# Performance work log

Measured on AMD Instinct MI355X. Metric: run time of the kernel, lower is better.

Reference implementation:

```python
import jax, jax.numpy as jnp
import numpy as np


def setup_inputs() -> dict:
    key = jax.random.key(0)
    k1, k2 = jax.random.split(key)
    B, C, H, W = 8, 64, 32, 32
    K = 8192
    x = jax.random.normal(k1, (B, C, H, W), dtype=jnp.float32)
    codebook = jax.random.normal(k2, (K, C), dtype=jnp.float32)
    return {"x": x, "codebook": codebook}


def reference(x, codebook):
    """Faithful JAX version of VQVAE.quantize().

    x:        [B, C, H, W] latent (output of pre_quant_conv)
    codebook: [K, C] embedding weight
    Returns (quant_out [B,C,H,W], commitment_loss, codebook_loss, indices [B,H,W]).
    """
    B, C, H, W = x.shape
    # [B, H, W, C] -> [B, N, C]
    xf = jnp.transpose(x, (0, 2, 3, 1)).reshape(B, H * W, C)

    # Squared pairwise distances (argmin of cdist == argmin of squared dist).
    x2 = jnp.sum(xf * xf, axis=-1, keepdims=True)            # [B, N, 1]
    e2 = jnp.sum(codebook * codebook, axis=-1)               # [K]
    xe = jnp.einsum('bnc,kc->bnk', xf, codebook)             # [B, N, K]
    d2 = x2 + e2[None, None, :] - 2.0 * xe                   # [B, N, K]
    idx = jnp.argmin(d2, axis=-1)                            # [B, N]

    quant = codebook[idx.reshape(-1)]                        # [B*N, C]
    xflat = xf.reshape(-1, C)                                # [B*N, C]

    commitment_loss = jnp.mean((jax.lax.stop_gradient(quant) - xflat) ** 2)
    codebook_loss = jnp.mean((quant - jax.lax.stop_gradient(xflat)) ** 2)

    # Straight-through estimator.
    quant_st = xflat + jax.lax.stop_gradient(quant - xflat)
    quant_out = jnp.transpose(quant_st.reshape(B, H, W, C), (0, 3, 1, 2))
    indices = idx.reshape(B, H, W)
    return quant_out, commitment_loss, codebook_loss, indices
```

## Files before the change

kernel.cpp:

```cpp
#include <hip/hip_runtime.h>


#define N_PTS   8192
#define K_CODES 8192
#define C_DIM   64
#define HWSZ    1024
#define QOUT_N  524288
#define SPLITS  32

#define WS_XS    0
#define WS_CBS   3145728
#define WS_E2H   6291456
#define WS_PACK  6324224
#define WS_PART  8421376

typedef __attribute__((ext_vector_type(8))) short short8;
typedef __attribute__((ext_vector_type(4))) float floatx4;

__device__ __forceinline__ unsigned short bf16_rne(float f) {
    unsigned u = __float_as_uint(f);
    return (unsigned short)((u + 0x7FFFu + ((u >> 16) & 1u)) >> 16);
}
__device__ __forceinline__ float bf16_val(unsigned short h) {
    return __uint_as_float(((unsigned)h) << 16);
}
__device__ __forceinline__ void split3(float v, unsigned short& h,
                                       unsigned short& m, unsigned short& l) {
    h = bf16_rne(v);
    float r1 = v - bf16_val(h);
    m = bf16_rne(r1);
    float r2 = r1 - bf16_val(m);
    l = bf16_rne(r2);
}
__device__ __forceinline__ void cp16(const void* g, void* l) {
    __builtin_amdgcn_global_load_lds(
        (const __attribute__((address_space(1))) void*)g,
        (__attribute__((address_space(3))) void*)l, 16, 0, 0);
}
__device__ __forceinline__ void cp4(const void* g, void* l) {
    __builtin_amdgcn_global_load_lds(
        (const __attribute__((address_space(1))) void*)g,
        (__attribute__((address_space(3))) void*)l, 4, 0, 0);
}

__global__ __launch_bounds__(256)
void vq_prep_kernel(const float* __restrict__ x,
                    const float* __restrict__ cb,
                    unsigned short* __restrict__ xS,
                    unsigned short* __restrict__ cbS,
                    float* __restrict__ e2h)
{
    const int bx  = blockIdx.x;
    const int tid = threadIdx.x;

    if (bx < 32) {
        const int k = bx * 256 + tid;
        const float* row = cb + k * C_DIM;
        float s = 0.0f;
        #pragma unroll
        for (int g = 0; g < 8; ++g) {
            float4 a = *(const float4*)(row + g * 8);
            float4 b = *(const float4*)(row + g * 8 + 4);
            float vv[8] = {a.x, a.y, a.z, a.w, b.x, b.y, b.z, b.w};
            unsigned short h8[8], m8[8], l8[8];
            #pragma unroll
            for (int j = 0; j < 8; ++j) {
                s = fmaf(vv[j], vv[j], s);
                split3(vv[j], h8[j], m8[j], l8[j]);
            }
            *(uint4*)(cbS + ((size_t)(0 * 8 + g) * 8192 + k) * 8) = *(const uint4*)h8;
            *(uint4*)(cbS + ((size_t)(1 * 8 + g) * 8192 + k) * 8) = *(const uint4*)m8;
            *(uint4*)(cbS + ((size_t)(2 * 8 + g) * 8192 + k) * 8) = *(const uint4*)l8;
        }
        e2h[k] = 0.5f * s;
    } else {
        const int u = bx - 32;
        const int b = u >> 3, g = u & 7;
        const float* xb = x + (size_t)(b * C_DIM + g * 8) * HWSZ;
        float v[4][8];
        #pragma unroll
        for (int cq = 0; cq < 8; ++cq) {
            float4 t4 = *(const float4*)(xb + cq * HWSZ + tid * 4);
            v[0][cq] = t4.x; v[1][cq] = t4.y; v[2][cq] = t4.z; v[3][cq] = t4.w;
        }
        #pragma unroll
        for (int j = 0; j < 4; ++j) {
            unsigned short h8[8], m8[8], l8[8];
            #pragma unroll
            for (int cq = 0; cq < 8; ++cq)
                split3(v[j][cq], h8[cq], m8[cq], l8[cq]);
            const size_t n = (size_t)b * 1024 + tid * 4 + j;
            *(uint4*)(xS + ((size_t)(0 * 8 + g) * 8192 + n) * 8) = *(const uint4*)h8;
            *(uint4*)(xS + ((size_t)(1 * 8 + g) * 8192 + n) * 8) = *(const uint4*)m8;
            *(uint4*)(xS + ((size_t)(2 * 8 + g) * 8192 + n) * 8) = *(const uint4*)l8;
        }
    }
}

#define SEG_SHORTS 512
#define BUF_SHORTS 12416

__device__ __forceinline__ void computeTileLDS(const short8 af[4][3][2],
                                               const unsigned short* __restrict__ bsrc,
                                               int tl, int quad, int col, int code,
                                               float bestv[4][4], int besti[4][4])
{
    short8 bf[3][2];
    #pragma unroll
    for (int p = 0; p < 3; ++p)
        #pragma unroll
        for (int s = 0; s < 2; ++s) {
            int seg = p * 8 + s * 4 + quad;
            bf[p][s] = *(const short8*)(bsrc + seg * SEG_SHORTS + (tl * 16 + col) * 8);
        }
    float me2 = -((const float*)(bsrc + 24 * SEG_SHORTS))[tl * 16 + col];

    floatx4 acc[4];
    #pragma unroll
    for (int t = 0; t < 4; ++t) acc[t] = (floatx4){me2, me2, me2, me2};

    #pragma unroll
    for (int s = 0; s < 2; ++s) {
        #pragma unroll
        for (int t = 0; t < 4; ++t)
            acc[t] = __builtin_amdgcn_mfma_f32_16x16x32_bf16(af[t][0][s], bf[0][s], acc[t], 0, 0, 0);
        #pragma unroll
        for (int t = 0; t < 4; ++t)
            acc[t] = __builtin_amdgcn_mfma_f32_16x16x32_bf16(af[t][0][s], bf[1][s], acc[t], 0, 0, 0);
        #pragma unroll
        for (int t = 0; t < 4; ++t)
            acc[t] = __builtin_amdgcn_mfma_f32_16x16x32_bf16(af[t][1][s], bf[0][s], acc[t], 0, 0, 0);
        #pragma unroll
        for (int t = 0; t < 4; ++t)
            acc[t] = __builtin_amdgcn_mfma_f32_16x16x32_bf16(af[t][0][s], bf[2][s], acc[t], 0, 0, 0);
        #pragma unroll
        for (int t = 0; t < 4; ++t)
            acc[t] = __builtin_amdgcn_mfma_f32_16x16x32_bf16(af[t][2][s], bf[0][s], acc[t], 0, 0, 0);
        #pragma unroll
        for (int t = 0; t < 4; ++t)
            acc[t] = __builtin_amdgcn_mfma_f32_16x16x32_bf16(af[t][1][s], bf[1][s], acc[t], 0, 0, 0);
    }

    #pragma unroll
    for (int t = 0; t < 4; ++t)
        #pragma unroll
        for (int r = 0; r < 4; ++r) {
            float sc = acc[t][r];
            bool gt = sc > bestv[t][r];
            bestv[t][r] = gt ? sc   : bestv[t][r];
            besti[t][r] = gt ? code : besti[t][r];
        }
}

__global__ __launch_bounds__(256, 2)
void vq_argmin_kernel(const unsigned short* __restrict__ xS,
                      const unsigned short* __restrict__ cbS,
                      const float* __restrict__ e2h,
                      unsigned long long* __restrict__ packedS)
{
    __shared__ __align__(16) unsigned short sBuf[2][BUF_SHORTS];

    const int tid   = threadIdx.x;
    const int lane  = tid & 63;
    const int w     = tid >> 6;
    const int col   = lane & 15;
    const int quad  = lane >> 4;
    const int mb    = blockIdx.x;
    const int split = blockIdx.y;
    const int m0    = mb * 256 + w * 64;
    const int nb0   = split * 256;

    short8 af[4][3][2];
    #pragma unroll
    for (int t = 0; t < 4; ++t) {
        int pt = m0 + t * 16 + col;
        #pragma unroll
        for (int p = 0; p < 3; ++p)
            #pragma unroll
            for (int s = 0; s < 2; ++s) {
                int g = s * 4 + quad;
                af[t][p][s] = *(const short8*)(xS + ((size_t)(p * 8 + g) * 8192 + pt) * 8);
            }
    }

    float bestv[4][4];
    int   besti[4][4];
    #pragma unroll
    for (int t = 0; t < 4; ++t)
        #pragma unroll
        for (int r = 0; r < 4; ++r) {
            bestv[t][r] = __uint_as_float(0xFF800000u);
            besti[t][r] = 0;
        }

    auto stage = [&](int k0, int buf) {
        unsigned short* dst = &sBuf[buf][0];
        #pragma unroll
        for (int i = 0; i < 6; ++i) {
            int f   = tid + i * 256;
            int seg = f >> 6;
            int l   = f & 63;
            cp16(cbS + ((size_t)seg * 8192 + k0 + l) * 8,
                 dst + seg * SEG_SHORTS + l * 8);
        }
        if (tid < 64)
            cp4(e2h + k0 + tid, (float*)(dst + 24 * SEG_SHORTS) + tid);
    };

    stage(nb0, 0);
    __syncthreads();

    for (int ch = 0; ch < 4; ++ch) {
        if (ch + 1 < 4) stage(nb0 + (ch + 1) * 64, (ch + 1) & 1);
        const unsigned short* bsrc = &sBuf[ch & 1][0];
        #pragma unroll
        for (int tl = 0; tl < 4; ++tl)
            computeTileLDS(af, bsrc, tl, quad, col,
                           nb0 + ch * 64 + tl * 16 + col, bestv, besti);
        __syncthreads();
    }

    unsigned long long* red = (unsigned long long*)&sBuf[0][0];
    #pragma unroll
    for (int t = 0; t < 4; ++t)
        #pragma unroll
        for (int r = 0; r < 4; ++r) {
            unsigned u = __float_as_uint(-bestv[t][r]);
            u = ((int)u < 0) ? ~u : (u | 0x80000000u);
            unsigned long long p = ((unsigned long long)u << 32) | (unsigned)besti[t][r];
            red[(w * 64 + t * 16 + quad * 4 + r) * 17 + col] = p;
        }
    __syncthreads();
    unsigned long long v = red[tid * 17];
    #pragma unroll
    for (int c = 1; c < 16; ++c) {
        unsigned long long q = red[tid * 17 + c];
        v = (q < v) ? q : v;
    }
    packedS[(size_t)split * N_PTS + mb * 256 + tid] = v;
}

__global__ __launch_bounds__(256)
void vq_gather_kernel(const float* __restrict__ x,
                      const float* __restrict__ cb,
                      const unsigned long long* __restrict__ packedS,
                      float* __restrict__ out,
                      float* __restrict__ part)
{
    __shared__ int sidx[64];
    const int tid  = threadIdx.x;
    const int lane = tid & 63;
    const int qd   = tid >> 6;
    const int n0   = blockIdx.x * 64;
    const int n    = n0 + lane;

    if (qd == 0) {
        unsigned long long v = packedS[n];
        #pragma unroll
        for (int s = 1; s < SPLITS; ++s) {
            unsigned long long q = packedS[(size_t)s * N_PTS + n];
            v = (q < v) ? q : v;
        }
        int idx = (int)(v & 0xFFFFFFFFull);
        sidx[lane] = idx;
        out[QOUT_N + 2 + n] = (float)idx;
    }
    __syncthreads();

    const int idx = sidx[lane];
    const int c0  = qd * 16;
    const int b   = n >> 10;
    const int hw  = n & 1023;
    const float* xb = x   + (size_t)b * (C_DIM * HWSZ) + hw;
    float*       ob = out + (size_t)b * (C_DIM * HWSZ) + hw;

    float s = 0.0f;
    #pragma unroll
    for (int c4 = 0; c4 < 4; ++c4) {
        float4 q = *(const float4*)(cb + (size_t)idx * C_DIM + c0 + c4 * 4);
        float qa[4] = {q.x, q.y, q.z, q.w};
        #pragma unroll
        for (int j = 0; j < 4; ++j) {
            int c = c0 + c4 * 4 + j;
            float xv = xb[c * HWSZ];
            float d  = qa[j] - xv;
            s = fmaf(d, d, s);
            ob[c * HWSZ] = xv + d;
        }
    }

    #pragma unroll
    for (int off = 32; off > 0; off >>= 1) s += __shfl_down(s, off, 64);
    if (lane == 0) part[blockIdx.x * 4 + qd] = s;
}

__global__ __launch_bounds__(256)
void vq_final_kernel(const float* __restrict__ part, float* __restrict__ out)
{
    __shared__ float w[4];
    float s = part[threadIdx.x] + part[threadIdx.x + 256];
    #pragma unroll
    for (int off = 32; off > 0; off >>= 1) s += __shfl_down(s, off, 64);
    if ((threadIdx.x & 63) == 0) w[threadIdx.x >> 6] = s;
    __syncthreads();
    if (threadIdx.x == 0) {
        float m = (w[0] + w[1] + w[2] + w[3]) * (1.0f / (float)QOUT_N);
        out[QOUT_N]     = m;
        out[QOUT_N + 1] = m;
    }
}

extern "C" void kernel_launch(void* const* d_in, const int* in_sizes, int n_in,
                              void* d_out, int out_size, void* d_ws, size_t ws_size,
                              hipStream_t stream)
{
    const float* x  = (const float*)d_in[0];
    const float* cb = (const float*)d_in[1];
    float* out = (float*)d_out;
    char*  ws  = (char*)d_ws;
    (void)ws_size;

    unsigned short* xS  = (unsigned short*)(ws + WS_XS);
    unsigned short* cbS = (unsigned short*)(ws + WS_CBS);
    float* e2h = (float*)(ws + WS_E2H);
    unsigned long long* packedS = (unsigned long long*)(ws + WS_PACK);
    float* part = (float*)(ws + WS_PART);

    vq_prep_kernel<<<96, 256, 0, stream>>>(x, cb, xS, cbS, e2h);
    vq_argmin_kernel<<<dim3(N_PTS / 256, SPLITS), 256, 0, stream>>>(xS, cbS, e2h, packedS);
    vq_gather_kernel<<<128, 256, 0, stream>>>(x, cb, packedS, out, part);
    vq_final_kernel<<<1, 256, 0, stream>>>(part, out);
}
```

Baseline: 103.8 us.

## Single-buffer codebook LDS staging and replace LDS reduction with wave shuffles

Replaces the double-buffered LDS staging of codebook chunks with a single buffer, loaded between two barriers after each chunk is computed. This halves LDS use per block so more blocks can be resident, at the cost of no longer overlapping chunk loads with MFMA compute. The final per-point argmin across the 16 columns now uses xor shuffles within the wave instead of an LDS scratch array and an extra barrier. Each lane writes the result for one point, computed from its column and quad.

```diff
diff --git a/kernel.cpp b/kernel.cpp
--- a/kernel.cpp
+++ b/kernel.cpp
@@ -158,7 +158,7 @@
                       const float* __restrict__ e2h,
                       unsigned long long* __restrict__ packedS)
 {
-    __shared__ __align__(16) unsigned short sBuf[2][BUF_SHORTS];
+    __shared__ __align__(16) unsigned short sBuf[BUF_SHORTS];
 
     const int tid   = threadIdx.x;
     const int lane  = tid & 63;
@@ -193,34 +193,35 @@
             besti[t][r] = 0;
         }
 
-    auto stage = [&](int k0, int buf) {
-        unsigned short* dst = &sBuf[buf][0];
+    auto stage = [&](int k0) {
         #pragma unroll
         for (int i = 0; i < 6; ++i) {
             int f   = tid + i * 256;
             int seg = f >> 6;
             int l   = f & 63;
             cp16(cbS + ((size_t)seg * 8192 + k0 + l) * 8,
-                 dst + seg * SEG_SHORTS + l * 8);
+                 sBuf + seg * SEG_SHORTS + l * 8);
         }
         if (tid < 64)
-            cp4(e2h + k0 + tid, (float*)(dst + 24 * SEG_SHORTS) + tid);
+            cp4(e2h + k0 + tid, (float*)(sBuf + 24 * SEG_SHORTS) + tid);
     };
 
-    stage(nb0, 0);
+    stage(nb0);
     __syncthreads();
 
     for (int ch = 0; ch < 4; ++ch) {
-        if (ch + 1 < 4) stage(nb0 + (ch + 1) * 64, (ch + 1) & 1);
-        const unsigned short* bsrc = &sBuf[ch & 1][0];
         #pragma unroll
         for (int tl = 0; tl < 4; ++tl)
-            computeTileLDS(af, bsrc, tl, quad, col,
+            computeTileLDS(af, sBuf, tl, quad, col,
                            nb0 + ch * 64 + tl * 16 + col, bestv, besti);
-        __syncthreads();
-    }
-
-    unsigned long long* red = (unsigned long long*)&sBuf[0][0];
+        if (ch + 1 < 4) {
+            __syncthreads();
+            stage(nb0 + (ch + 1) * 64);
+            __syncthreads();
+        }
+    }
+
+    unsigned long long own = 0;
     #pragma unroll
     for (int t = 0; t < 4; ++t)
         #pragma unroll
@@ -228,16 +229,15 @@
             unsigned u = __float_as_uint(-bestv[t][r]);
             u = ((int)u < 0) ? ~u : (u | 0x80000000u);
             unsigned long long p = ((unsigned long long)u << 32) | (unsigned)besti[t][r];
-            red[(w * 64 + t * 16 + quad * 4 + r) * 17 + col] = p;
-        }
-    __syncthreads();
-    unsigned long long v = red[tid * 17];
-    #pragma unroll
-    for (int c = 1; c < 16; ++c) {
-        unsigned long long q = red[tid * 17 + c];
-        v = (q < v) ? q : v;
-    }
-    packedS[(size_t)split * N_PTS + mb * 256 + tid] = v;
+            #pragma unroll
+            for (int msk = 1; msk < 16; msk <<= 1) {
+                unsigned long long q = __shfl_xor(p, msk, 64);
+                p = (q < p) ? q : p;
+            }
+            own = (col == t * 4 + r) ? p : own;
+        }
+    const int mpt = m0 + (col >> 2) * 16 + quad * 4 + (col & 3);
+    packedS[(size_t)split * N_PTS + mpt] = own;
 }
 
 __global__ __launch_bounds__(256)
```

Measured after the change: 109.0 us. +5.0%, slower.

## Switch argmin to 32x32x16 MFMA tiles with split accumulators and shuffle reduction

Applied to the files above, without the earlier changes.

Rewrites the distance argmin kernel to use 32x32x16 bf16 MFMA instead of 16x16x32. Each wave now owns 32 points and each block 128 points and 512 codes, so there are 16 splits instead of 32. Two independent accumulators break the MFMA dependency chain. The LDS-based final min reduction is replaced by wave shuffles. The larger MFMA shape cuts LDS B-fragment reads per FLOP, and fewer splits shrink the partial-result buffer. The costs are more registers and a longer per-block serial loop.

```diff
diff --git a/kernel.cpp b/kernel.cpp
--- a/kernel.cpp
+++ b/kernel.cpp
@@ -6,16 +6,16 @@
 #define C_DIM   64
 #define HWSZ    1024
 #define QOUT_N  524288
-#define SPLITS  32
+#define SPLITS  16
 
 #define WS_XS    0
 #define WS_CBS   3145728
 #define WS_E2H   6291456
 #define WS_PACK  6324224
-#define WS_PART  8421376
-
-typedef __attribute__((ext_vector_type(8))) short short8;
-typedef __attribute__((ext_vector_type(4))) float floatx4;
+#define WS_PART  7372800
+
+typedef __attribute__((ext_vector_type(8)))  short short8;
+typedef __attribute__((ext_vector_type(16))) float floatx16;
 
 __device__ __forceinline__ unsigned short bf16_rne(float f) {
     unsigned u = __float_as_uint(f);
@@ -100,58 +100,6 @@
 #define SEG_SHORTS 512
 #define BUF_SHORTS 12416
 
-__device__ __forceinline__ void computeTileLDS(const short8 af[4][3][2],
-                                               const unsigned short* __restrict__ bsrc,
-                                               int tl, int quad, int col, int code,
-                                               float bestv[4][4], int besti[4][4])
-{
-    short8 bf[3][2];
-    #pragma unroll
-    for (int p = 0; p < 3; ++p)
-        #pragma unroll
-        for (int s = 0; s < 2; ++s) {
-            int seg = p * 8 + s * 4 + quad;
-            bf[p][s] = *(const short8*)(bsrc + seg * SEG_SHORTS + (tl * 16 + col) * 8);
-        }
-    float me2 = -((const float*)(bsrc + 24 * SEG_SHORTS))[tl * 16 + col];
-
-    floatx4 acc[4];
-    #pragma unroll
-    for (int t = 0; t < 4; ++t) acc[t] = (floatx4){me2, me2, me2, me2};
-
-    #pragma unroll
-    for (int s = 0; s < 2; ++s) {
-        #pragma unroll
-        for (int t = 0; t < 4; ++t)
-            acc[t] = __builtin_amdgcn_mfma_f32_16x16x32_bf16(af[t][0][s], bf[0][s], acc[t], 0, 0, 0);
-        #pragma unroll
-        for (int t = 0; t < 4; ++t)
-            acc[t] = __builtin_amdgcn_mfma_f32_16x16x32_bf16(af[t][0][s], bf[1][s], acc[t], 0, 0, 0);
-        #pragma unroll
-        for (int t = 0; t < 4; ++t)
-            acc[t] = __builtin_amdgcn_mfma_f32_16x16x32_bf16(af[t][1][s], bf[0][s], acc[t], 0, 0, 0);
-        #pragma unroll
-        for (int t = 0; t < 4; ++t)
-            acc[t] = __builtin_amdgcn_mfma_f32_16x16x32_bf16(af[t][0][s], bf[2][s], acc[t], 0, 0, 0);
-        #pragma unroll
-        for (int t = 0; t < 4; ++t)
-            acc[t] = __builtin_amdgcn_mfma_f32_16x16x32_bf16(af[t][2][s], bf[0][s], acc[t], 0, 0, 0);
-        #pragma unroll
-        for (int t = 0; t < 4; ++t)
-            acc[t] = __builtin_amdgcn_mfma_f32_16x16x32_bf16(af[t][1][s], bf[1][s], acc[t], 0, 0, 0);
-    }
-
-    #pragma unroll
-    for (int t = 0; t < 4; ++t)
-        #pragma unroll
-        for (int r = 0; r < 4; ++r) {
-            float sc = acc[t][r];
-            bool gt = sc > bestv[t][r];
-            bestv[t][r] = gt ? sc   : bestv[t][r];
-            besti[t][r] = gt ? code : besti[t][r];
-        }
-}
-
 __global__ __launch_bounds__(256, 2)
 void vq_argmin_kernel(const unsigned short* __restrict__ xS,
                       const unsigned short* __restrict__ cbS,
@@ -163,35 +111,32 @@
     const int tid   = threadIdx.x;
     const int lane  = tid & 63;
     const int w     = tid >> 6;
-    const int col   = lane & 15;
-    const int quad  = lane >> 4;
+    const int l31   = lane & 31;
+    const int half  = lane >> 5;
     const int mb    = blockIdx.x;
     const int split = blockIdx.y;
-    const int m0    = mb * 256 + w * 64;
-    const int nb0   = split * 256;
-
-    short8 af[4][3][2];
-    #pragma unroll
-    for (int t = 0; t < 4; ++t) {
-        int pt = m0 + t * 16 + col;
+    const int m0    = mb * 128 + w * 32;
+    const int nb0   = split * 512;
+
+    short8 af[3][4];
+    {
+        const int pt = m0 + l31;
         #pragma unroll
         for (int p = 0; p < 3; ++p)
             #pragma unroll
-            for (int s = 0; s < 2; ++s) {
-                int g = s * 4 + quad;
-                af[t][p][s] = *(const short8*)(xS + ((size_t)(p * 8 + g) * 8192 + pt) * 8);
+            for (int s = 0; s < 4; ++s) {
+                int g = s * 2 + half;
+                af[p][s] = *(const short8*)(xS + ((size_t)(p * 8 + g) * 8192 + pt) * 8);
             }
     }
 
-    float bestv[4][4];
-    int   besti[4][4];
-    #pragma unroll
-    for (int t = 0; t < 4; ++t)
-        #pragma unroll
-        for (int r = 0; r < 4; ++r) {
-            bestv[t][r] = __uint_as_float(0xFF800000u);
-            besti[t][r] = 0;
-        }
+    float bestv[16];
+    int   besti[16];
+    #pragma unroll
+    for (int r = 0; r < 16; ++r) {
+        bestv[r] = __uint_as_float(0xFF800000u);
+        besti[r] = 0;
+    }
 
     auto stage = [&](int k0, int buf) {
         unsigned short* dst = &sBuf[buf][0];
@@ -210,34 +155,63 @@
     stage(nb0, 0);
     __syncthreads();
 
-    for (int ch = 0; ch < 4; ++ch) {
-        if (ch + 1 < 4) stage(nb0 + (ch + 1) * 64, (ch + 1) & 1);
+    for (int ch = 0; ch < 8; ++ch) {
+        if (ch + 1 < 8) stage(nb0 + (ch + 1) * 64, (ch + 1) & 1);
         const unsigned short* bsrc = &sBuf[ch & 1][0];
-        #pragma unroll
-        for (int tl = 0; tl < 4; ++tl)
-            computeTileLDS(af, bsrc, tl, quad, col,
-                           nb0 + ch * 64 + tl * 16 + col, bestv, besti);
+        const float* e2s = (const float*)(bsrc + 24 * SEG_SHORTS);
+
+        #pragma unroll
+        for (int ntl = 0; ntl < 2; ++ntl) {
+            const int lc   = ntl * 32 + l31;
+            const int code = nb0 + ch * 64 + lc;
+            const float me2 = -e2s[lc];
+
+            floatx16 accA, accB;
+            #pragma unroll
+            for (int r = 0; r < 16; ++r) { accA[r] = me2; accB[r] = 0.0f; }
+
+            #pragma unroll
+            for (int s = 0; s < 4; ++s) {
+                const int g = s * 2 + half;
+                short8 b0 = *(const short8*)(bsrc + (0 * 8 + g) * SEG_SHORTS + lc * 8);
+                short8 b1 = *(const short8*)(bsrc + (1 * 8 + g) * SEG_SHORTS + lc * 8);
+                short8 b2 = *(const short8*)(bsrc + (2 * 8 + g) * SEG_SHORTS + lc * 8);
+                accA = __builtin_amdgcn_mfma_f32_32x32x16_bf16(af[0][s], b0, accA, 0, 0, 0);
+                accB = __builtin_amdgcn_mfma_f32_32x32x16_bf16(af[0][s], b1, accB, 0, 0, 0);
+                accA = __builtin_amdgcn_mfma_f32_32x32x16_bf16(af[1][s], b0, accA, 0, 0, 0);
+                accB = __builtin_amdgcn_mfma_f32_32x32x16_bf16(af[0][s], b2, accB, 0, 0, 0);
+                accA = __builtin_amdgcn_mfma_f32_32x32x16_bf16(af[2][s], b0, accA, 0, 0, 0);
+                accB = __builtin_amdgcn_mfma_f32_32x32x16_bf16(af[1][s], b1, accB, 0, 0, 0);
+            }
+
+            #pragma unroll
+            for (int r = 0; r < 16; ++r) {
+                float sc = accA[r] + accB[r];
+                bool gt = sc > bestv[r];
+                bestv[r] = gt ? sc   : bestv[r];
+                besti[r] = gt ? code : besti[r];
+            }
+        }
         __syncthreads();
     }
 
-    unsigned long long* red = (unsigned long long*)&sBuf[0][0];
-    #pragma unroll
-    for (int t = 0; t < 4; ++t)
-        #pragma unroll
-        for (int r = 0; r < 4; ++r) {
-            unsigned u = __float_as_uint(-bestv[t][r]);
-            u = ((int)u < 0) ? ~u : (u | 0x80000000u);
-            unsigned long long p = ((unsigned long long)u << 32) | (unsigned)besti[t][r];
-            red[(w * 64 + t * 16 + quad * 4 + r) * 17 + col] = p;
-        }
-    __syncthreads();
-    unsigned long long v = red[tid * 17];
-    #pragma unroll
-    for (int c = 1; c < 16; ++c) {
-        unsigned long long q = red[tid * 17 + c];
-        v = (q < v) ? q : v;
-    }
-    packedS[(size_t)split * N_PTS + mb * 256 + tid] = v;
+    unsigned long long own = 0;
+    #pragma unroll
+    for (int r = 0; r < 16; ++r) {
+        unsigned u = __float_as_uint(-bestv[r]);
+        u = ((int)u < 0) ? ~u : (u | 0x80000000u);
+        unsigned long long p = ((unsigned long long)u << 32) | (unsigned)besti[r];
+        #pragma unroll
+        for (int msk = 1; msk < 32; msk <<= 1) {
+            unsigned long long q = __shfl_xor(p, msk, 64);
+            p = (q < p) ? q : p;
+        }
+        own = (l31 == r) ? p : own;
+    }
+    if (l31 < 16) {
+        const int row = (l31 & 3) + 8 * (l31 >> 2) + 4 * half;
+        packedS[(size_t)split * N_PTS + m0 + row] = own;
+    }
 }
 
 __global__ __launch_bounds__(256)
@@ -327,7 +301,7 @@
     float* part = (float*)(ws + WS_PART);
 
     vq_prep_kernel<<<96, 256, 0, stream>>>(x, cb, xS, cbS, e2h);
-    vq_argmin_kernel<<<dim3(N_PTS / 256, SPLITS), 256, 0, stream>>>(xS, cbS, e2h, packedS);
+    vq_argmin_kernel<<<dim3(64, SPLITS), 256, 0, stream>>>(xS, cbS, e2h, packedS);
     vq_gather_kernel<<<128, 256, 0, stream>>>(x, cb, packedS, out, part);
     vq_final_kernel<<<1, 256, 0, stream>>>(part, out);
 }
```

Result: slower. 116.3 us (+12.0%).
